# Performance work log

Hardware: AMD Instinct MI355X
Metric: run time of the kernel (lower is better)

## Reference

```python
import jax, jax.numpy as jnp
import numpy as np

H = 1024
NH = 16
HD = H // NH  # 64


def setup_inputs() -> dict:
    key = jax.random.key(0)
    ks = jax.random.split(key, 7)
    s = 1.0 / np.sqrt(H)
    return {
        "hidden_states": jax.random.normal(ks[0], (4, 2048, H), dtype=jnp.float32),
        "Wq": jax.random.normal(ks[1], (H, H), dtype=jnp.float32) * s,
        "bq": jnp.zeros((H,), dtype=jnp.float32),
        "Wk": jax.random.normal(ks[2], (H, H), dtype=jnp.float32) * s,
        "bk": jnp.zeros((H,), dtype=jnp.float32),
        "Wv": jax.random.normal(ks[3], (H, H), dtype=jnp.float32) * s,
        "bv": jnp.zeros((H,), dtype=jnp.float32),
    }


def _split_heads(x):
    # [B,S,H] -> [B,NH,S,HD]
    b, s, _ = x.shape
    return x.reshape(b, s, NH, HD).transpose(0, 2, 1, 3)


def reference(hidden_states, Wq, bq, Wk, bk, Wv, bv):
    q = _split_heads(hidden_states @ Wq + bq)
    k = _split_heads(hidden_states @ Wk + bk)
    v = _split_heads(hidden_states @ Wv + bv)
    scores = jnp.einsum("bhqd,bhkd->bhqk", q, k) / jnp.sqrt(jnp.float32(HD))
    probs = jax.nn.softmax(scores, axis=-1)  # dropout p=0 (eval) -> identity
    ctx = jnp.einsum("bhqk,bhkd->bhqd", probs, v)
    b, _, s, _ = ctx.shape
    return ctx.transpose(0, 2, 1, 3).reshape(b, s, H)
```

## Files before the change

### kernel.cpp

```cpp
#include <hip/hip_runtime.h>
#include <hip/hip_bf16.h>

#define BB  4
#define SS  2048
#define HH  1024
#define NHH 16
#define HDD 64

typedef unsigned short u16;
typedef unsigned int   u32;
using bf16x8 = __attribute__((ext_vector_type(8))) short;
using f32x4  = __attribute__((ext_vector_type(4))) float;

__device__ __forceinline__ u16 f2b(float f) {
    union { float f; u32 u; } x; x.f = f;
    return (u16)((x.u + 0x7fffu + ((x.u >> 16) & 1u)) >> 16);
}
__device__ __forceinline__ u32 pk2b(float lo, float hi) {
    union { float f; u32 u; } a, b; a.f = lo; b.f = hi;
    return __builtin_amdgcn_perm(b.u + 0x8000u, a.u + 0x8000u, 0x07060302u);
}

__device__ __forceinline__ void gload16(const u16* g, u16* l) {
    __builtin_amdgcn_global_load_lds(
        (const __attribute__((address_space(1))) void*)g,
        (__attribute__((address_space(3))) void*)l, 16, 0, 0);
}

__global__ __launch_bounds__(256) void conv(
    const float* __restrict__ X,
    const float* __restrict__ Wq, const float* __restrict__ Wk,
    const float* __restrict__ Wv,
    u16* __restrict__ Xb, u16* __restrict__ Wt)
{
    const int bid = blockIdx.x;
    const int t = threadIdx.x;
    if (bid < 4096) {
        const int i = bid * 256 + t;
        float4 a = ((const float4*)X)[i * 2];
        float4 b = ((const float4*)X)[i * 2 + 1];
        ushort4 s0, s1;
        s0.x = f2b(a.x); s0.y = f2b(a.y); s0.z = f2b(a.z); s0.w = f2b(a.w);
        s1.x = f2b(b.x); s1.y = f2b(b.y); s1.z = f2b(b.z); s1.w = f2b(b.w);
        ((ushort4*)Xb)[i * 2] = s0;
        ((ushort4*)Xb)[i * 2 + 1] = s1;
        return;
    }
    const int idx = bid - 4096;
    const int z = idx >> 10, rem = idx & 1023;
    const int k0 = (rem >> 5) * 32, n0 = (rem & 31) * 32;
    const float* W = (z == 0) ? Wq : (z == 1) ? Wk : Wv;
    u16* out = Wt + (size_t)z * HH * HH;
    __shared__ float T[32][33];
    {
        const int kl = t >> 3, n4 = (t & 7) * 4;
        float4 v = *(const float4*)&W[(size_t)(k0 + kl) * HH + n0 + n4];
        T[n4 + 0][kl] = v.x; T[n4 + 1][kl] = v.y;
        T[n4 + 2][kl] = v.z; T[n4 + 3][kl] = v.w;
    }
    __syncthreads();
    {
        const int nl = t >> 3, k4 = (t & 7) * 4;
        ushort4 s;
        s.x = f2b(T[nl][k4 + 0]); s.y = f2b(T[nl][k4 + 1]);
        s.z = f2b(T[nl][k4 + 2]); s.w = f2b(T[nl][k4 + 3]);
        *(ushort4*)&out[(size_t)(n0 + nl) * HH + k0 + k4] = s;
    }
}

__global__ __launch_bounds__(256) void qkv_gemm(
    const u16* __restrict__ Xb, const u16* __restrict__ Wtb,
    const float* __restrict__ bq, const float* __restrict__ bk,
    const float* __restrict__ bv,
    u16* __restrict__ Qw, u16* __restrict__ Kw, u16* __restrict__ Vw)
{
    const int z  = blockIdx.z;
    const float* bias = (z == 0) ? bq : (z == 1) ? bk : bv;
    const int m0 = blockIdx.x * 128, n0 = blockIdx.y * 128;

    __shared__ __align__(16) u16 Xs[128 * 64];
    __shared__ __align__(16) u16 Ws[128 * 64];

    const int t = threadIdx.x;
    const int w = t >> 6, lane = t & 63, lr = lane & 15, quad = lane >> 4;
    const int l3 = lane >> 3, c7 = lane & 7;
    const int cl = (c7 ^ l3) * 8;
    const int wm = w >> 1, wn = w & 1;

    const u16* Wtz = Wtb + (size_t)z * HH * HH;

    f32x4 acc[4][4];
    #pragma unroll
    for (int i = 0; i < 4; i++)
        #pragma unroll
        for (int j = 0; j < 4; j++) acc[i][j] = f32x4{0.f, 0.f, 0.f, 0.f};

    for (int k0 = 0; k0 < HH; k0 += 64) {
        #pragma unroll
        for (int e = 0; e < 4; e++) {
            const int r = w * 32 + e * 8 + l3;
            gload16(&Xb [(size_t)(m0 + r) * HH + k0 + cl], &Xs[(w * 32 + e * 8) * 64]);
            gload16(&Wtz[(size_t)(n0 + r) * HH + k0 + cl], &Ws[(w * 32 + e * 8) * 64]);
        }
        __syncthreads();

        #pragma unroll
        for (int kc = 0; kc < 2; kc++) {
            bf16x8 af[4], bfr[4];
            const int ph = ((kc * 4 + quad) ^ c7) * 8;
            #pragma unroll
            for (int mi = 0; mi < 4; mi++)
                af[mi] = *(const bf16x8*)&Xs[(wm * 64 + mi * 16 + lr) * 64 + ph];
            #pragma unroll
            for (int ni = 0; ni < 4; ni++)
                bfr[ni] = *(const bf16x8*)&Ws[(wn * 64 + ni * 16 + lr) * 64 + ph];
            if (z != 2) {
                #pragma unroll
                for (int mi = 0; mi < 4; mi++)
                    #pragma unroll
                    for (int ni = 0; ni < 4; ni++)
                        acc[mi][ni] = __builtin_amdgcn_mfma_f32_16x16x32_bf16(
                            bfr[ni], af[mi], acc[mi][ni], 0, 0, 0);
            } else {
                #pragma unroll
                for (int mi = 0; mi < 4; mi++)
                    #pragma unroll
                    for (int ni = 0; ni < 4; ni++)
                        acc[mi][ni] = __builtin_amdgcn_mfma_f32_16x16x32_bf16(
                            af[mi], bfr[ni], acc[mi][ni], 0, 0, 0);
            }
        }
        __syncthreads();
    }

    if (z != 2) {
        u16* dst = (z == 0) ? Qw : Kw;
        const float cs = (z == 0) ? 0.18033688011112042f : 1.0f;
        #pragma unroll
        for (int mi = 0; mi < 4; mi++) {
            const int sg = m0 + wm * 64 + mi * 16 + lr;
            const int b = sg >> 11, s = sg & 2047;
            #pragma unroll
            for (int ni = 0; ni < 4; ni++) {
                const int nb = n0 + wn * 64 + ni * 16 + quad * 4;
                const int h = nb >> 6, d0 = nb & 63;
                float4 bb4 = *(const float4*)&bias[nb];
                ushort4 vs;
                vs.x = f2b((acc[mi][ni][0] + bb4.x) * cs);
                vs.y = f2b((acc[mi][ni][1] + bb4.y) * cs);
                vs.z = f2b((acc[mi][ni][2] + bb4.z) * cs);
                vs.w = f2b((acc[mi][ni][3] + bb4.w) * cs);
                *(ushort4*)&dst[((size_t)(b * NHH + h) * SS + s) * HDD + d0] = vs;
            }
        }
    } else {
        #pragma unroll
        for (int mi = 0; mi < 4; mi++)
            #pragma unroll
            for (int ni = 0; ni < 4; ni++) {
                const int mb = m0 + wm * 64 + mi * 16 + quad * 4;
                const int b = mb >> 11, s0 = mb & 2047;
                const int n = n0 + wn * 64 + ni * 16 + lr;
                const int h = n >> 6, d = n & 63;
                const float bv4 = bias[n];
                ushort4 vs;
                vs.x = f2b(acc[mi][ni][0] + bv4);
                vs.y = f2b(acc[mi][ni][1] + bv4);
                vs.z = f2b(acc[mi][ni][2] + bv4);
                vs.w = f2b(acc[mi][ni][3] + bv4);
                *(ushort4*)&Vw[((size_t)(b * NHH + h) * HDD + d) * SS + s0] = vs;
            }
    }
}

__global__ __launch_bounds__(512) void attn(
    const u16* __restrict__ Qb, const u16* __restrict__ Kb,
    const u16* __restrict__ Vtb, float* __restrict__ Out)
{
    const int bid = blockIdx.x;
    const int hh = bid & 63, qt = bid >> 6;
    const int b = hh >> 4, h = hh & 15;
    const size_t hb = (size_t)hh * SS * HDD;

    __shared__ __align__(16) u16 Ks[2][64 * 64];
    __shared__ __align__(16) u16 Vs[2][64 * 64];
    __shared__ __align__(16) u16 Ps[8][16 * 72];

    const int t = threadIdx.x;
    const int w = t >> 6, lane = t & 63, lr = lane & 15, quad = lane >> 4;
    const int l3 = lane >> 3, c7 = lane & 7;
    const int cl = (c7 ^ l3) * 8;

    bf16x8 qa[2];
    #pragma unroll
    for (int kc = 0; kc < 2; kc++)
        qa[kc] = *(const bf16x8*)&Qb[hb + (size_t)(qt * 128 + w * 16 + lr) * HDD
                                     + kc * 32 + quad * 8];

    {
        const int r8 = w * 8 + l3;
        gload16(&Kb [hb + (size_t)r8 * HDD + cl], &Ks[0][w * 8 * 64]);
        gload16(&Vtb[hb + (size_t)r8 * SS + cl],  &Vs[0][w * 8 * 64]);
    }
    __syncthreads();

    float lsum = 0.f;
    f32x4 oc[4];
    #pragma unroll
    for (int ni = 0; ni < 4; ni++) oc[ni] = f32x4{0.f, 0.f, 0.f, 0.f};

    for (int kt = 0; kt < SS / 64; kt++) {
        const int bb = kt & 1;
        if (kt + 1 < SS / 64) {
            const int r8 = w * 8 + l3;
            gload16(&Kb [hb + (size_t)((kt + 1) * 64 + r8) * HDD + cl],
                    &Ks[bb ^ 1][w * 8 * 64]);
            gload16(&Vtb[hb + (size_t)r8 * SS + (kt + 1) * 64 + cl],
                    &Vs[bb ^ 1][w * 8 * 64]);
        }

        f32x4 sc4[4];
        #pragma unroll
        for (int ni = 0; ni < 4; ni++) sc4[ni] = f32x4{0.f, 0.f, 0.f, 0.f};
        #pragma unroll
        for (int kc = 0; kc < 2; kc++) {
            const int ph = ((kc * 4 + quad) ^ c7) * 8;
            #pragma unroll
            for (int ni = 0; ni < 4; ni++) {
                bf16x8 kf = *(const bf16x8*)&Ks[bb][(ni * 16 + lr) * 64 + ph];
                sc4[ni] = __builtin_amdgcn_mfma_f32_16x16x32_bf16(kf, qa[kc], sc4[ni], 0, 0, 0);
            }
        }

        #pragma unroll
        for (int ni = 0; ni < 4; ni++) {
            float pv0 = __builtin_amdgcn_exp2f(sc4[ni][0]);
            float pv1 = __builtin_amdgcn_exp2f(sc4[ni][1]);
            float pv2 = __builtin_amdgcn_exp2f(sc4[ni][2]);
            float pv3 = __builtin_amdgcn_exp2f(sc4[ni][3]);
            lsum += (pv0 + pv1) + (pv2 + pv3);
            uint2 pk;
            pk.x = pk2b(pv0, pv1);
            pk.y = pk2b(pv2, pv3);
            *(uint2*)&Ps[w][lr * 72 + ni * 16 + quad * 4] = pk;
        }

        bf16x8 pa[2];
        #pragma unroll
        for (int kc = 0; kc < 2; kc++)
            pa[kc] = *(const bf16x8*)&Ps[w][lr * 72 + kc * 32 + quad * 8];

        #pragma unroll
        for (int kc = 0; kc < 2; kc++) {
            const int ph = ((kc * 4 + quad) ^ c7) * 8;
            #pragma unroll
            for (int ni = 0; ni < 4; ni++) {
                bf16x8 vf = *(const bf16x8*)&Vs[bb][(ni * 16 + lr) * 64 + ph];
                oc[ni] = __builtin_amdgcn_mfma_f32_16x16x32_bf16(pa[kc], vf, oc[ni], 0, 0, 0);
            }
        }
        __syncthreads();
    }

    lsum += __shfl_xor(lsum, 16);
    lsum += __shfl_xor(lsum, 32);
    const float linv = 1.0f / lsum;

    #pragma unroll
    for (int ni = 0; ni < 4; ni++)
        #pragma unroll
        for (int r = 0; r < 4; r++) {
            const float inv = __shfl(linv, quad * 4 + r);
            const int rq = qt * 128 + w * 16 + quad * 4 + r;
            Out[((size_t)(b * SS + rq)) * HH + h * HDD + ni * 16 + lr] =
                oc[ni][r] * inv;
        }
}

extern "C" void kernel_launch(void* const* d_in, const int* in_sizes, int n_in,
                              void* d_out, int out_size, void* d_ws, size_t ws_size,
                              hipStream_t stream) {
    const float* X  = (const float*)d_in[0];
    const float* Wq = (const float*)d_in[1];
    const float* bq = (const float*)d_in[2];
    const float* Wk = (const float*)d_in[3];
    const float* bk = (const float*)d_in[4];
    const float* Wv = (const float*)d_in[5];
    const float* bv = (const float*)d_in[6];
    float* Out = (float*)d_out;

    const size_t elems = (size_t)BB * SS * HH;
    u16* Qw = (u16*)d_ws;
    u16* Kw = Qw + elems;
    u16* Vw = Kw + elems;
    u16* Xb = (u16*)d_out;
    u16* Wt = Xb + elems;

    conv<<<dim3(4096 + 3072), 256, 0, stream>>>(X, Wq, Wk, Wv, Xb, Wt);
    qkv_gemm<<<dim3(64, 8, 3), 256, 0, stream>>>(Xb, Wt, bq, bk, bv, Qw, Kw, Vw);
    attn<<<dim3(1024), 512, 0, stream>>>(Qw, Kw, Vw, Out);
}
```

Before: 255.7 us.

## Double-buffer QKV GEMM K-tiles and precompute swizzled LDS offsets in attention

The QKV GEMM now splits each 64-wide K step into two 32-wide halves held in double-buffered LDS, so the next half is prefetched while MFMAs run on the current one. It uses a new XOR swizzle layout with precomputed fragment offsets. The attention loop is unrolled by two with compile-time buffer indices and precomputed K/V and P offsets, and the P scratch gets a swizzled 64-stride layout in place of padding. The aim is to hide global-load latency and cut address arithmetic, at the cost of twice as many barriers per K step in the GEMM and more registers.

Result: no change. 258.0 us (+0.9%).

```diff
diff --git a/kernel.cpp b/kernel.cpp
--- a/kernel.cpp
+++ b/kernel.cpp
@@ -78,16 +78,28 @@
     const float* bias = (z == 0) ? bq : (z == 1) ? bk : bv;
     const int m0 = blockIdx.x * 128, n0 = blockIdx.y * 128;
 
-    __shared__ __align__(16) u16 Xs[128 * 64];
-    __shared__ __align__(16) u16 Ws[128 * 64];
+    __shared__ __align__(16) u16 Xs[2][4096];
+    __shared__ __align__(16) u16 Ws[2][4096];
 
     const int t = threadIdx.x;
     const int w = t >> 6, lane = t & 63, lr = lane & 15, quad = lane >> 4;
-    const int l3 = lane >> 3, c7 = lane & 7;
-    const int cl = (c7 ^ l3) * 8;
     const int wm = w >> 1, wn = w & 1;
 
+    const int llog = (lane & 7) ^ (lane >> 3);
+    const int mIdx = (lane >> 3) * 2 + (llog >> 2);
+    const int kcol = (llog & 3) * 8;
+
     const u16* Wtz = Wtb + (size_t)z * HH * HH;
+    const u16* gx = Xb  + (size_t)(m0 + w * 32 + mIdx) * HH + kcol;
+    const u16* gw = Wtz + (size_t)(n0 + w * 32 + mIdx) * HH + kcol;
+
+    int aoff[4], boff[4];
+    const int fch = ((((lr & 1) << 2) | quad) ^ (lr >> 1)) << 3;
+    #pragma unroll
+    for (int i = 0; i < 4; i++) {
+        aoff[i] = (wm * 32 + i * 8 + (lr >> 1)) * 64 + fch;
+        boff[i] = (wn * 32 + i * 8 + (lr >> 1)) * 64 + fch;
+    }
 
     f32x4 acc[4][4];
     #pragma unroll
@@ -95,41 +107,43 @@
         #pragma unroll
         for (int j = 0; j < 4; j++) acc[i][j] = f32x4{0.f, 0.f, 0.f, 0.f};
 
-    for (int k0 = 0; k0 < HH; k0 += 64) {
-        #pragma unroll
-        for (int e = 0; e < 4; e++) {
-            const int r = w * 32 + e * 8 + l3;
-            gload16(&Xb [(size_t)(m0 + r) * HH + k0 + cl], &Xs[(w * 32 + e * 8) * 64]);
-            gload16(&Wtz[(size_t)(n0 + r) * HH + k0 + cl], &Ws[(w * 32 + e * 8) * 64]);
-        }
+    #define QKV_PREFETCH(buf, k0v)                                          \
+        { _Pragma("unroll")                                                 \
+          for (int e = 0; e < 2; e++) {                                     \
+              gload16(gx + (size_t)e * 16 * HH + (k0v), &Xs[buf][(w*16+e*8)*64]); \
+              gload16(gw + (size_t)e * 16 * HH + (k0v), &Ws[buf][(w*16+e*8)*64]); \
+          } }
+
+    #define QKV_COMPUTE(buf)                                                \
+        { bf16x8 af[4], bfr[4];                                             \
+          _Pragma("unroll")                                                 \
+          for (int mi = 0; mi < 4; mi++) af[mi]  = *(const bf16x8*)&Xs[buf][aoff[mi]]; \
+          _Pragma("unroll")                                                 \
+          for (int ni = 0; ni < 4; ni++) bfr[ni] = *(const bf16x8*)&Ws[buf][boff[ni]]; \
+          if (z != 2) {                                                     \
+              _Pragma("unroll")                                             \
+              for (int mi = 0; mi < 4; mi++)                                \
+                  _Pragma("unroll")                                         \
+                  for (int ni = 0; ni < 4; ni++)                            \
+                      acc[mi][ni] = __builtin_amdgcn_mfma_f32_16x16x32_bf16(\
+                          bfr[ni], af[mi], acc[mi][ni], 0, 0, 0);           \
+          } else {                                                          \
+              _Pragma("unroll")                                             \
+              for (int mi = 0; mi < 4; mi++)                                \
+                  _Pragma("unroll")                                         \
+                  for (int ni = 0; ni < 4; ni++)                            \
+                      acc[mi][ni] = __builtin_amdgcn_mfma_f32_16x16x32_bf16(\
+                          af[mi], bfr[ni], acc[mi][ni], 0, 0, 0);           \
+          } }
+
+    QKV_PREFETCH(0, 0)
+    __syncthreads();
+    for (int kt2 = 0; kt2 < 16; kt2++) {
+        QKV_PREFETCH(1, kt2 * 64 + 32)
+        QKV_COMPUTE(0)
         __syncthreads();
-
-        #pragma unroll
-        for (int kc = 0; kc < 2; kc++) {
-            bf16x8 af[4], bfr[4];
-            const int ph = ((kc * 4 + quad) ^ c7) * 8;
-            #pragma unroll
-            for (int mi = 0; mi < 4; mi++)
-                af[mi] = *(const bf16x8*)&Xs[(wm * 64 + mi * 16 + lr) * 64 + ph];
-            #pragma unroll
-            for (int ni = 0; ni < 4; ni++)
-                bfr[ni] = *(const bf16x8*)&Ws[(wn * 64 + ni * 16 + lr) * 64 + ph];
-            if (z != 2) {
-                #pragma unroll
-                for (int mi = 0; mi < 4; mi++)
-                    #pragma unroll
-                    for (int ni = 0; ni < 4; ni++)
-                        acc[mi][ni] = __builtin_amdgcn_mfma_f32_16x16x32_bf16(
-                            bfr[ni], af[mi], acc[mi][ni], 0, 0, 0);
-            } else {
-                #pragma unroll
-                for (int mi = 0; mi < 4; mi++)
-                    #pragma unroll
-                    for (int ni = 0; ni < 4; ni++)
-                        acc[mi][ni] = __builtin_amdgcn_mfma_f32_16x16x32_bf16(
-                            af[mi], bfr[ni], acc[mi][ni], 0, 0, 0);
-            }
-        }
+        if (kt2 < 15) QKV_PREFETCH(0, kt2 * 64 + 64)
+        QKV_COMPUTE(1)
         __syncthreads();
     }
 
@@ -182,9 +196,9 @@
     const int b = hh >> 4, h = hh & 15;
     const size_t hb = (size_t)hh * SS * HDD;
 
-    __shared__ __align__(16) u16 Ks[2][64 * 64];
-    __shared__ __align__(16) u16 Vs[2][64 * 64];
-    __shared__ __align__(16) u16 Ps[8][16 * 72];
+    __shared__ __align__(16) u16 Ks[2][4096];
+    __shared__ __align__(16) u16 Vs[2][4096];
+    __shared__ __align__(16) u16 Ps[8][1024];
 
     const int t = threadIdx.x;
     const int w = t >> 6, lane = t & 63, lr = lane & 15, quad = lane >> 4;
@@ -197,11 +211,27 @@
         qa[kc] = *(const bf16x8*)&Qb[hb + (size_t)(qt * 128 + w * 16 + lr) * HDD
                                      + kc * 32 + quad * 8];
 
-    {
-        const int r8 = w * 8 + l3;
-        gload16(&Kb [hb + (size_t)r8 * HDD + cl], &Ks[0][w * 8 * 64]);
-        gload16(&Vtb[hb + (size_t)r8 * SS + cl],  &Vs[0][w * 8 * 64]);
-    }
+    int kvoff[2][4];
+    #pragma unroll
+    for (int kc = 0; kc < 2; kc++)
+        #pragma unroll
+        for (int ni = 0; ni < 4; ni++)
+            kvoff[kc][ni] = (ni * 16 + lr) * 64 + (((kc * 4 + quad) ^ c7) << 3);
+    int pwoff[4], proff[2];
+    #pragma unroll
+    for (int ni = 0; ni < 4; ni++)
+        pwoff[ni] = lr * 64 + ((((ni * 2 + (quad >> 1)) ^ (lr & 7)) << 3)
+                               | ((quad & 1) << 2));
+    #pragma unroll
+    for (int kc = 0; kc < 2; kc++)
+        proff[kc] = lr * 64 + (((kc * 4 + quad) ^ (lr & 7)) << 3);
+
+    const int r8 = w * 8 + l3;
+    const u16* gk = Kb  + hb + (size_t)r8 * HDD + cl;
+    const u16* gv = Vtb + hb + (size_t)r8 * SS + cl;
+
+    gload16(gk, &Ks[0][w * 512]);
+    gload16(gv, &Vs[0][w * 512]);
     __syncthreads();
 
     float lsum = 0.f;
@@ -209,29 +239,21 @@
     #pragma unroll
     for (int ni = 0; ni < 4; ni++) oc[ni] = f32x4{0.f, 0.f, 0.f, 0.f};
 
-    for (int kt = 0; kt < SS / 64; kt++) {
-        const int bb = kt & 1;
-        if (kt + 1 < SS / 64) {
-            const int r8 = w * 8 + l3;
-            gload16(&Kb [hb + (size_t)((kt + 1) * 64 + r8) * HDD + cl],
-                    &Ks[bb ^ 1][w * 8 * 64]);
-            gload16(&Vtb[hb + (size_t)r8 * SS + (kt + 1) * 64 + cl],
-                    &Vs[bb ^ 1][w * 8 * 64]);
+    auto tile = [&](int kt, const int bc, bool pf) {
+        if (pf) {
+            gload16(gk + (size_t)(kt + 1) * 4096, &Ks[bc ^ 1][w * 512]);
+            gload16(gv + (size_t)(kt + 1) * 64,   &Vs[bc ^ 1][w * 512]);
         }
-
         f32x4 sc4[4];
         #pragma unroll
         for (int ni = 0; ni < 4; ni++) sc4[ni] = f32x4{0.f, 0.f, 0.f, 0.f};
         #pragma unroll
-        for (int kc = 0; kc < 2; kc++) {
-            const int ph = ((kc * 4 + quad) ^ c7) * 8;
+        for (int kc = 0; kc < 2; kc++)
             #pragma unroll
             for (int ni = 0; ni < 4; ni++) {
-                bf16x8 kf = *(const bf16x8*)&Ks[bb][(ni * 16 + lr) * 64 + ph];
+                bf16x8 kf = *(const bf16x8*)&Ks[bc][kvoff[kc][ni]];
                 sc4[ni] = __builtin_amdgcn_mfma_f32_16x16x32_bf16(kf, qa[kc], sc4[ni], 0, 0, 0);
             }
-        }
-
         #pragma unroll
         for (int ni = 0; ni < 4; ni++) {
             float pv0 = __builtin_amdgcn_exp2f(sc4[ni][0]);
@@ -242,24 +264,25 @@
             uint2 pk;
             pk.x = pk2b(pv0, pv1);
             pk.y = pk2b(pv2, pv3);
-            *(uint2*)&Ps[w][lr * 72 + ni * 16 + quad * 4] = pk;
+            *(uint2*)&Ps[w][pwoff[ni]] = pk;
         }
-
         bf16x8 pa[2];
         #pragma unroll
         for (int kc = 0; kc < 2; kc++)
-            pa[kc] = *(const bf16x8*)&Ps[w][lr * 72 + kc * 32 + quad * 8];
-
-        #pragma unroll
-        for (int kc = 0; kc < 2; kc++) {
-            const int ph = ((kc * 4 + quad) ^ c7) * 8;
+            pa[kc] = *(const bf16x8*)&Ps[w][proff[kc]];
+        #pragma unroll
+        for (int kc = 0; kc < 2; kc++)
             #pragma unroll
             for (int ni = 0; ni < 4; ni++) {
-                bf16x8 vf = *(const bf16x8*)&Vs[bb][(ni * 16 + lr) * 64 + ph];
+                bf16x8 vf = *(const bf16x8*)&Vs[bc][kvoff[kc][ni]];
                 oc[ni] = __builtin_amdgcn_mfma_f32_16x16x32_bf16(pa[kc], vf, oc[ni], 0, 0, 0);
             }
-        }
         __syncthreads();
+    };
+
+    for (int kt2 = 0; kt2 < 16; kt2++) {
+        tile(2 * kt2,     0, true);
+        tile(2 * kt2 + 1, 1, kt2 < 15);
     }
 
     lsum += __shfl_xor(lsum, 16);
```
